# Kernel tuning notes

Hardware: AMD Instinct MI355X
Metric: run time of the kernel (lower is better)

The kernel has to match this reference:

```python
import jax, jax.numpy as jnp
import numpy as np

Q_LEN, KV_LEN, N_HEADS, HEAD_DIM = 2048, 4096, 16, 64
NEG_INF = -1e9


def _causal_prefix_mask(q_len, kv_len):
    # query i (global position prefix+i) may attend to keys j <= prefix + i
    prefix = kv_len - q_len
    i = jnp.arange(q_len)[:, None]
    j = jnp.arange(kv_len)[None, :]
    allowed = j <= (prefix + i)
    return jnp.where(allowed, 0.0, NEG_INF).astype(jnp.float32)[None, None]  # [1,1,q,kv]


def setup_inputs() -> dict:
    key = jax.random.key(0)
    kq, kk, kv = jax.random.split(key, 3)
    query = jax.random.normal(kq, (1, N_HEADS, Q_LEN, HEAD_DIM), dtype=jnp.float32)
    k = jax.random.normal(kk, (1, N_HEADS, KV_LEN, HEAD_DIM), dtype=jnp.float32)
    v = jax.random.normal(kv, (1, N_HEADS, KV_LEN, HEAD_DIM), dtype=jnp.float32)
    attn_mask = _causal_prefix_mask(Q_LEN, KV_LEN)
    return {"query": query, "key": k, "value": v, "attn_mask": attn_mask}


def reference(query, key, value, attn_mask):
    # Equivalent math of SlicedFusedSDPA.forward: chunked causal SDPA with
    # online-softmax merge == one full masked softmax attention.
    # scale=None -> 1/sqrt(head_dim); dropout_p=0; is_causal=True encoded in attn_mask.
    scale = 1.0 / np.sqrt(query.shape[-1]).astype(np.float32)
    scores = jnp.einsum('bhqd,bhkd->bhqk', query, key) * scale + attn_mask  # [B,H,Q,KV]
    probs = jax.nn.softmax(scores, axis=-1)
    out = jnp.einsum('bhqk,bhkd->bhqd', probs, value)
    return out.astype(query.dtype)
```

## Files before the change

kernel.cpp:

```cpp
#include <hip/hip_runtime.h>
#include <hip/hip_bf16.h>

#define NH 16
#define QL 2048
#define KVL 4096
#define DH 64
#define PREFIX (KVL - QL)
#define NT 64
#define TUS 8192
#define NS 2
#define SCALE 0.18033688011112043f

typedef __attribute__((ext_vector_type(8))) _Float16 f16x8;
typedef __attribute__((ext_vector_type(8))) short short8;
typedef __attribute__((ext_vector_type(4))) float f32x4;
typedef __attribute__((ext_vector_type(16))) float f32x16;
typedef unsigned int u32;

static __device__ __forceinline__ float exp2_fast(float x) {
    float r; asm("v_exp_f32 %0, %1" : "=v"(r) : "v"(x)); return r;
}
static __device__ __forceinline__ u32 pkrtz(float lo, float hi) {
    u32 r; asm("v_cvt_pkrtz_f16_f32 %0, %1, %2" : "=v"(r) : "v"(lo), "v"(hi)); return r;
}
static __device__ __forceinline__ void plswap(u32& x, u32& y) {
    asm("v_permlane32_swap_b32 %0, %1" : "+v"(x), "+v"(y));
}
#define MFMAH(a, b, c) __builtin_amdgcn_mfma_f32_32x32x16_f16(a, b, c, 0, 0, 0)

static __device__ __forceinline__ ushort f2bf(float x) {
    union { float f; u32 u; } v; v.f = x;
    u32 r = v.u + 0x7fffu + ((v.u >> 16) & 1u);
    return (ushort)(r >> 16);
}
static __device__ __forceinline__ float bf2f(ushort h) {
    union { u32 u; float f; } v; v.u = ((u32)h) << 16;
    return v.f;
}

__global__ void convK2(const float* __restrict__ K, ushort* __restrict__ ws) {
    const int gid  = blockIdx.x * 256 + threadIdx.x;
    const int lane = gid & 63;
    const int fidx = (gid >> 6) & 7;
    const int tile = (gid >> 9) & 63;
    const int h    = gid >> 15;
    const int lq = lane & 31, hi = lane >> 5;
    const int t = fidx >> 2, ks = fidx & 3;
    const int kv = tile * 64 + t * 32 + lq;
    const float* src = K + ((size_t)h * KVL + kv) * DH + ks * 16 + hi * 8;
    const float4 a = *(const float4*)src;
    const float4 b = *(const float4*)(src + 4);
    const float v[8] = {a.x, a.y, a.z, a.w, b.x, b.y, b.z, b.w};
    f16x8 o;
    #pragma unroll
    for (int j = 0; j < 8; ++j) o[j] = (_Float16)v[j];
    *(f16x8*)(ws + (size_t)(h * NT + tile) * TUS + fidx * 512 + lane * 8) = o;
}

__global__ void convV2(const float* __restrict__ V, ushort* __restrict__ ws) {
    const int gid  = blockIdx.x * 256 + threadIdx.x;
    const int lane = gid & 63;
    const int fidx = (gid >> 6) & 7;
    const int tile = (gid >> 9) & 63;
    const int h    = gid >> 15;
    const int lq = lane & 31, hi = lane >> 5;
    const int dt = fidx >> 2, ks = fidx & 3;
    const int d  = dt * 32 + lq;
    const float* src = V + ((size_t)h * KVL + tile * 64 + ks * 16 + hi * 8) * DH + d;
    f16x8 o;
    #pragma unroll
    for (int j = 0; j < 8; ++j) o[j] = (_Float16)src[j * DH];
    *(f16x8*)(ws + (size_t)(h * NT + tile) * TUS + 4096 + fidx * 512 + lane * 8) = o;
}

__global__ __launch_bounds__(256, 2)
void sdpa_main(const float* __restrict__ Q, const ushort* __restrict__ ws,
               float* __restrict__ part)
{
    const int tid  = threadIdx.x;
    const int lane = tid & 63;
    const int w    = tid >> 6;
    const int lq   = lane & 31;
    const int hi   = lane >> 5;

    const int bid = blockIdx.x;
    const int xcd = bid & 7;
    const int j   = bid >> 3;
    const int h   = xcd * 2 + (j & 1);
    const int qwA = j >> 1;
    const int qw  = (w & 1) ? (63 - qwA) : qwA;
    const int sp  = w >> 1;
    const int qb  = qw * 32;

    const int ntt = (PREFIX + qb + 32 + 63) >> 6;
    const int t0  = (ntt * sp) / NS;
    const int t1  = (ntt * (sp + 1)) / NS;

    f16x8 qh[4], ql[4];
    {
        const float* qp = Q + ((size_t)h * QL + qb + lq) * DH + hi * 8;
        #pragma unroll
        for (int ks = 0; ks < 4; ++ks) {
            const float4 a = *(const float4*)(qp + ks * 16);
            const float4 b = *(const float4*)(qp + ks * 16 + 4);
            const float v[8] = {a.x, a.y, a.z, a.w, b.x, b.y, b.z, b.w};
            #pragma unroll
            for (int jj = 0; jj < 8; ++jj) {
                const float x = v[jj] * SCALE;
                const _Float16 xh = (_Float16)x;
                qh[ks][jj] = xh;
                ql[ks][jj] = (_Float16)(x - (float)xh);
            }
        }
    }

    f32x16 oacc[2];
    #pragma unroll
    for (int dt = 0; dt < 2; ++dt)
        #pragma unroll
        for (int r = 0; r < 16; ++r) oacc[dt][r] = 0.f;
    float m = 0.0f, lsum = 0.f;

    const ushort* tb = ws + (size_t)h * NT * TUS + (size_t)t0 * TUS;

    for (int it = t0; it < t1; ++it, tb += TUS) {
        f16x8 kf[8], vf[8];
        #pragma unroll
        for (int f = 0; f < 8; ++f) kf[f] = *(const f16x8*)(tb + f * 512 + lane * 8);
        #pragma unroll
        for (int f = 0; f < 8; ++f) vf[f] = *(const f16x8*)(tb + 4096 + f * 512 + lane * 8);

        f32x16 sT[2];
        #pragma unroll
        for (int t = 0; t < 2; ++t)
            #pragma unroll
            for (int r = 0; r < 16; ++r) sT[t][r] = 0.f;

        __builtin_amdgcn_s_setprio(1);
        #pragma unroll
        for (int ks = 0; ks < 4; ++ks) {
            sT[0] = MFMAH(kf[ks],     qh[ks], sT[0]);
            sT[1] = MFMAH(kf[4 + ks], qh[ks], sT[1]);
            sT[0] = MFMAH(kf[ks],     ql[ks], sT[0]);
            sT[1] = MFMAH(kf[4 + ks], ql[ks], sT[1]);
        }
        __builtin_amdgcn_s_setprio(0);

        const int kv0 = it * 64;
        if (kv0 + 64 > PREFIX + qb) {
            const int kvlim = PREFIX + qb + lq - kv0;
            #pragma unroll
            for (int t = 0; t < 2; ++t)
                #pragma unroll
                for (int r = 0; r < 16; ++r) {
                    const int kvl = t * 32 + (r & 3) + 8 * (r >> 2) + 4 * hi;
                    if (kvl > kvlim) sT[t][r] = -1e30f;
                }
        }

        float mx = sT[0][0];
        #pragma unroll
        for (int t = 0; t < 2; ++t)
            #pragma unroll
            for (int r = 0; r < 16; ++r) mx = fmaxf(mx, sT[t][r]);
        mx = fmaxf(mx, __shfl_xor(mx, 32));
        if (__any(mx > m + 8.0f)) {
            const float mn  = fmaxf(m, mx);
            const float fsc = exp2_fast(m - mn);
            lsum *= fsc;
            #pragma unroll
            for (int dt = 0; dt < 2; ++dt)
                #pragma unroll
                for (int r = 0; r < 16; ++r) oacc[dt][r] *= fsc;
            m = mn;
        }
        float rs = 0.f;
        #pragma unroll
        for (int t = 0; t < 2; ++t)
            #pragma unroll
            for (int r = 0; r < 16; ++r) {
                const float p = exp2_fast(sT[t][r] - m);
                sT[t][r] = p;
                rs += p;
            }
        lsum += rs;

        f16x8 pb[4];
        #pragma unroll
        for (int t = 0; t < 2; ++t) {
            u32 x0 = pkrtz(sT[t][0],  sT[t][1]);
            u32 x1 = pkrtz(sT[t][2],  sT[t][3]);
            u32 y0 = pkrtz(sT[t][4],  sT[t][5]);
            u32 y1 = pkrtz(sT[t][6],  sT[t][7]);
            u32 x2 = pkrtz(sT[t][8],  sT[t][9]);
            u32 x3 = pkrtz(sT[t][10], sT[t][11]);
            u32 y2 = pkrtz(sT[t][12], sT[t][13]);
            u32 y3 = pkrtz(sT[t][14], sT[t][15]);
            plswap(x0, y0); plswap(x1, y1);
            plswap(x2, y2); plswap(x3, y3);
            union { u32 u[4]; f16x8 v; } p0, p1;
            p0.u[0] = x0; p0.u[1] = x1; p0.u[2] = y0; p0.u[3] = y1;
            p1.u[0] = x2; p1.u[1] = x3; p1.u[2] = y2; p1.u[3] = y3;
            pb[t * 2 + 0] = p0.v;
            pb[t * 2 + 1] = p1.v;
        }

        __builtin_amdgcn_s_setprio(1);
        #pragma unroll
        for (int ks = 0; ks < 4; ++ks) {
            oacc[0] = MFMAH(vf[ks],     pb[ks], oacc[0]);
            oacc[1] = MFMAH(vf[4 + ks], pb[ks], oacc[1]);
        }
        __builtin_amdgcn_s_setprio(0);
    }

    const float ltot = lsum + __shfl_xor(lsum, 32);
    float* pr = part + ((size_t)(sp * NH + h) * QL + qb + lq) * 68;
    #pragma unroll
    for (int dt = 0; dt < 2; ++dt)
        #pragma unroll
        for (int a = 0; a < 4; ++a) {
            f32x4 o;
            #pragma unroll
            for (int jj = 0; jj < 4; ++jj) o[jj] = oacc[dt][a * 4 + jj];
            *(f32x4*)(pr + dt * 32 + a * 8 + hi * 4) = o;
        }
    if (hi == 0) { pr[64] = m; pr[65] = ltot; }
}

__global__ void combine2(const float* __restrict__ part, float* __restrict__ O) {
    const int row = blockIdx.x * 4 + (threadIdx.x >> 6);
    const int d   = threadIdx.x & 63;
    const float* p0 = part + (size_t)row * 68;
    const float* p1 = part + ((size_t)NH * QL + row) * 68;
    const float m0 = p0[64], l0 = p0[65];
    const float m1 = p1[64], l1 = p1[65];
    const float M  = fmaxf(m0, m1);
    const float w0 = exp2f(m0 - M), w1 = exp2f(m1 - M);
    O[(size_t)row * DH + d] = (w0 * p0[d] + w1 * p1[d]) / (w0 * l0 + w1 * l1);
}

#define QT 64
#define KBf 32
#define KSTR 72
#define VSTR 40
#define PSTR 40
#define SCALE_E 0.125f

__global__ __launch_bounds__(256, 2)
void sdpa_fallback(const float* __restrict__ Q, const float* __restrict__ K,
                   const float* __restrict__ V, float* __restrict__ O)
{
    __shared__ ushort sKh[KBf][KSTR];
    __shared__ ushort sKl[KBf][KSTR];
    __shared__ ushort sVt[DH][VSTR];
    __shared__ ushort sPf[4][16][PSTR];

    const int tid  = threadIdx.x;
    const int lane = tid & 63;
    const int w    = tid >> 6;
    const int h    = blockIdx.y;
    const int q0   = blockIdx.x * QT;
    const int qb   = q0 + w * 16;
    const int lrow = lane & 15;
    const int lgrp = lane >> 4;

    short8 qh[2], ql[2];
    {
        const float* qp = Q + ((size_t)h * QL + (qb + lrow)) * DH;
        #pragma unroll
        for (int dh = 0; dh < 2; ++dh) {
            const int d0 = dh * 32 + lgrp * 8;
            #pragma unroll
            for (int jj = 0; jj < 8; ++jj) {
                float x = qp[d0 + jj] * SCALE_E;
                ushort hb = f2bf(x);
                qh[dh][jj] = (short)hb;
                ql[dh][jj] = (short)f2bf(x - bf2f(hb));
            }
        }
    }

    f32x4 oacc[4];
    float m_r[4], l_r[4];
    #pragma unroll
    for (int n = 0; n < 4; ++n) { oacc[n][0]=0.f; oacc[n][1]=0.f; oacc[n][2]=0.f; oacc[n][3]=0.f; }
    #pragma unroll
    for (int r = 0; r < 4; ++r) { m_r[r] = -1e30f; l_r[r] = 0.f; }

    const int nkv = min(KVL, PREFIX + q0 + QT);

    for (int kv0 = 0; kv0 < nkv; kv0 += KBf) {
        __syncthreads();
        {
            const int r  = tid >> 3;
            const int d0 = (tid & 7) * 8;
            const float* kp = K + ((size_t)h * KVL + (kv0 + r)) * DH + d0;
            const float* vp = V + ((size_t)h * KVL + (kv0 + r)) * DH + d0;
            short8 vh, vl;
            #pragma unroll
            for (int jj = 0; jj < 8; ++jj) {
                float x = kp[jj];
                ushort hb = f2bf(x);
                vh[jj] = (short)hb;
                vl[jj] = (short)f2bf(x - bf2f(hb));
            }
            *(short8*)&sKh[r][d0] = vh;
            *(short8*)&sKl[r][d0] = vl;
            #pragma unroll
            for (int jj = 0; jj < 8; ++jj)
                sVt[d0 + jj][r] = f2bf(vp[jj]);
        }
        __syncthreads();

        f32x4 s[2];
        #pragma unroll
        for (int t = 0; t < 2; ++t) { s[t][0]=0.f; s[t][1]=0.f; s[t][2]=0.f; s[t][3]=0.f; }
        #pragma unroll
        for (int t = 0; t < 2; ++t) {
            #pragma unroll
            for (int dh = 0; dh < 2; ++dh) {
                const short8 kh = *(const short8*)&sKh[t*16 + lrow][dh*32 + lgrp*8];
                const short8 kl = *(const short8*)&sKl[t*16 + lrow][dh*32 + lgrp*8];
                s[t] = __builtin_amdgcn_mfma_f32_16x16x32_bf16(qh[dh], kh, s[t], 0, 0, 0);
                s[t] = __builtin_amdgcn_mfma_f32_16x16x32_bf16(qh[dh], kl, s[t], 0, 0, 0);
                s[t] = __builtin_amdgcn_mfma_f32_16x16x32_bf16(ql[dh], kh, s[t], 0, 0, 0);
            }
        }

        if (kv0 + KBf > PREFIX + qb) {
            #pragma unroll
            for (int t = 0; t < 2; ++t)
                #pragma unroll
                for (int r = 0; r < 4; ++r) {
                    const int kv = kv0 + t*16 + lrow;
                    const int q  = qb + lgrp*4 + r;
                    if (kv > PREFIX + q) s[t][r] = -1e30f;
                }
        }

        float tmax[4];
        #pragma unroll
        for (int r = 0; r < 4; ++r) tmax[r] = fmaxf(s[0][r], s[1][r]);
        #pragma unroll
        for (int off = 1; off <= 8; off <<= 1)
            #pragma unroll
            for (int r = 0; r < 4; ++r) tmax[r] = fmaxf(tmax[r], __shfl_xor(tmax[r], off, 64));

        float f[4];
        #pragma unroll
        for (int r = 0; r < 4; ++r) {
            const float mn = fmaxf(m_r[r], tmax[r]);
            f[r] = __expf(m_r[r] - mn);
            m_r[r] = mn;
        }
        #pragma unroll
        for (int t = 0; t < 2; ++t)
            #pragma unroll
            for (int r = 0; r < 4; ++r) s[t][r] = __expf(s[t][r] - m_r[r]);

        float rs[4];
        #pragma unroll
        for (int r = 0; r < 4; ++r) rs[r] = s[0][r] + s[1][r];
        #pragma unroll
        for (int off = 1; off <= 8; off <<= 1)
            #pragma unroll
            for (int r = 0; r < 4; ++r) rs[r] += __shfl_xor(rs[r], off, 64);
        #pragma unroll
        for (int r = 0; r < 4; ++r) l_r[r] = l_r[r] * f[r] + rs[r];
        #pragma unroll
        for (int n = 0; n < 4; ++n)
            #pragma unroll
            for (int r = 0; r < 4; ++r) oacc[n][r] *= f[r];

        #pragma unroll
        for (int t = 0; t < 2; ++t)
            #pragma unroll
            for (int r = 0; r < 4; ++r)
                sPf[w][lgrp*4 + r][t*16 + lrow] = f2bf(s[t][r]);
        asm volatile("s_waitcnt lgkmcnt(0)" ::: "memory");
        __builtin_amdgcn_sched_barrier(0);

        const short8 pa = *(const short8*)&sPf[w][lrow][lgrp*8];
        #pragma unroll
        for (int n = 0; n < 4; ++n) {
            const short8 vb = *(const short8*)&sVt[n*16 + lrow][lgrp*8];
            oacc[n] = __builtin_amdgcn_mfma_f32_16x16x32_bf16(pa, vb, oacc[n], 0, 0, 0);
        }
    }

    float inv[4];
    #pragma unroll
    for (int r = 0; r < 4; ++r) inv[r] = 1.0f / l_r[r];
    float* op = O + ((size_t)h * QL + qb) * DH;
    #pragma unroll
    for (int n = 0; n < 4; ++n)
        #pragma unroll
        for (int r = 0; r < 4; ++r)
            op[(lgrp*4 + r) * DH + n*16 + lrow] = oacc[n][r] * inv[r];
}

extern "C" void kernel_launch(void* const* d_in, const int* in_sizes, int n_in,
                              void* d_out, int out_size, void* d_ws, size_t ws_size,
                              hipStream_t stream) {
    const float* Q = (const float*)d_in[0];
    const float* K = (const float*)d_in[1];
    const float* V = (const float*)d_in[2];
    float* O = (float*)d_out;
    const size_t KVWS = (size_t)NH * NT * TUS * 2;
    const size_t PART = (size_t)NH * QL * 68 * 4;

    if (ws_size >= KVWS + NS * PART) {
        ushort* wsKV = (ushort*)d_ws;
        float*  part = (float*)((char*)d_ws + KVWS);
        hipLaunchKernelGGL(convK2, dim3(2048), dim3(256), 0, stream, K, wsKV);
        hipLaunchKernelGGL(convV2, dim3(2048), dim3(256), 0, stream, V, wsKV);
        hipLaunchKernelGGL(sdpa_main, dim3(512), dim3(256), 0, stream, Q, wsKV, part);
        hipLaunchKernelGGL(combine2, dim3(8192), dim3(256), 0, stream, part, O);
    } else {
        hipLaunchKernelGGL(sdpa_fallback, dim3(32, 16), dim3(256), 0, stream, Q, K, V, O);
    }
}
```

Baseline: 71.69 us.

## Split KV range four ways, merge conversion kernels, tree-reduce softmax max/sum

Templates the main attention kernel on the number of KV splits and launches four splits (1024 blocks) instead of two when workspace allows, with a generalized combine kernel. The K and V fp16 conversion kernels are merged into one launch. Row max and sum reductions become pairwise trees to shorten dependency chains. More splits raise parallelism and balance on the GPU but increase partial-result traffic and combine cost.

Result: slower. 76.34 us (+6.5%).

```diff
diff --git a/kernel.cpp b/kernel.cpp
--- a/kernel.cpp
+++ b/kernel.cpp
@@ -8,7 +8,6 @@
 #define PREFIX (KVL - QL)
 #define NT 64
 #define TUS 8192
-#define NS 2
 #define SCALE 0.18033688011112043f
 
 typedef __attribute__((ext_vector_type(8))) _Float16 f16x8;
@@ -38,41 +37,37 @@
     return v.f;
 }
 
-__global__ void convK2(const float* __restrict__ K, ushort* __restrict__ ws) {
-    const int gid  = blockIdx.x * 256 + threadIdx.x;
+__global__ void convKV(const float* __restrict__ K, const float* __restrict__ V,
+                       ushort* __restrict__ ws) {
+    const int half = blockIdx.x >> 11;
+    const int gid  = (blockIdx.x & 2047) * 256 + threadIdx.x;
     const int lane = gid & 63;
     const int fidx = (gid >> 6) & 7;
     const int tile = (gid >> 9) & 63;
     const int h    = gid >> 15;
     const int lq = lane & 31, hi = lane >> 5;
-    const int t = fidx >> 2, ks = fidx & 3;
-    const int kv = tile * 64 + t * 32 + lq;
-    const float* src = K + ((size_t)h * KVL + kv) * DH + ks * 16 + hi * 8;
-    const float4 a = *(const float4*)src;
-    const float4 b = *(const float4*)(src + 4);
-    const float v[8] = {a.x, a.y, a.z, a.w, b.x, b.y, b.z, b.w};
     f16x8 o;
-    #pragma unroll
-    for (int j = 0; j < 8; ++j) o[j] = (_Float16)v[j];
-    *(f16x8*)(ws + (size_t)(h * NT + tile) * TUS + fidx * 512 + lane * 8) = o;
-}
-
-__global__ void convV2(const float* __restrict__ V, ushort* __restrict__ ws) {
-    const int gid  = blockIdx.x * 256 + threadIdx.x;
-    const int lane = gid & 63;
-    const int fidx = (gid >> 6) & 7;
-    const int tile = (gid >> 9) & 63;
-    const int h    = gid >> 15;
-    const int lq = lane & 31, hi = lane >> 5;
-    const int dt = fidx >> 2, ks = fidx & 3;
-    const int d  = dt * 32 + lq;
-    const float* src = V + ((size_t)h * KVL + tile * 64 + ks * 16 + hi * 8) * DH + d;
-    f16x8 o;
-    #pragma unroll
-    for (int j = 0; j < 8; ++j) o[j] = (_Float16)src[j * DH];
-    *(f16x8*)(ws + (size_t)(h * NT + tile) * TUS + 4096 + fidx * 512 + lane * 8) = o;
-}
-
+    if (half == 0) {
+        const int t = fidx >> 2, ks = fidx & 3;
+        const int kv = tile * 64 + t * 32 + lq;
+        const float* src = K + ((size_t)h * KVL + kv) * DH + ks * 16 + hi * 8;
+        const float4 a = *(const float4*)src;
+        const float4 b = *(const float4*)(src + 4);
+        const float v[8] = {a.x, a.y, a.z, a.w, b.x, b.y, b.z, b.w};
+        #pragma unroll
+        for (int j = 0; j < 8; ++j) o[j] = (_Float16)v[j];
+        *(f16x8*)(ws + (size_t)(h * NT + tile) * TUS + fidx * 512 + lane * 8) = o;
+    } else {
+        const int dt = fidx >> 2, ks = fidx & 3;
+        const int d  = dt * 32 + lq;
+        const float* src = V + ((size_t)h * KVL + tile * 64 + ks * 16 + hi * 8) * DH + d;
+        #pragma unroll
+        for (int j = 0; j < 8; ++j) o[j] = (_Float16)src[j * DH];
+        *(f16x8*)(ws + (size_t)(h * NT + tile) * TUS + 4096 + fidx * 512 + lane * 8) = o;
+    }
+}
+
+template<int NSPLIT>
 __global__ __launch_bounds__(256, 2)
 void sdpa_main(const float* __restrict__ Q, const ushort* __restrict__ ws,
                float* __restrict__ part)
@@ -86,15 +81,22 @@
     const int bid = blockIdx.x;
     const int xcd = bid & 7;
     const int j   = bid >> 3;
-    const int h   = xcd * 2 + (j & 1);
-    const int qwA = j >> 1;
-    const int qw  = (w & 1) ? (63 - qwA) : qwA;
-    const int sp  = w >> 1;
-    const int qb  = qw * 32;
+    int h, qwA, sp;
+    if constexpr (NSPLIT == 4) {
+        h   = xcd * 2 + (j & 1);
+        qwA = j >> 2;
+        sp  = ((j >> 1) & 1) * 2 + (w >> 1);
+    } else {
+        h   = xcd * 2 + (j & 1);
+        qwA = j >> 1;
+        sp  = w >> 1;
+    }
+    const int qw = (w & 1) ? (63 - qwA) : qwA;
+    const int qb = qw * 32;
 
     const int ntt = (PREFIX + qb + 32 + 63) >> 6;
-    const int t0  = (ntt * sp) / NS;
-    const int t1  = (ntt * (sp + 1)) / NS;
+    const int t0  = (ntt * sp) / NSPLIT;
+    const int t1  = (ntt * (sp + 1)) / NSPLIT;
 
     f16x8 qh[4], ql[4];
     {
@@ -158,12 +160,14 @@
                 }
         }
 
-        float mx = sT[0][0];
-        #pragma unroll
-        for (int t = 0; t < 2; ++t)
-            #pragma unroll
-            for (int r = 0; r < 16; ++r) mx = fmaxf(mx, sT[t][r]);
-        mx = fmaxf(mx, __shfl_xor(mx, 32));
+        float tmx[16];
+        #pragma unroll
+        for (int i = 0; i < 16; ++i) tmx[i] = fmaxf(sT[0][i], sT[1][i]);
+        #pragma unroll
+        for (int s = 8; s > 0; s >>= 1)
+            #pragma unroll
+            for (int i = 0; i < s; ++i) tmx[i] = fmaxf(tmx[i], tmx[i + s]);
+        float mx = fmaxf(tmx[0], __shfl_xor(tmx[0], 32));
         if (__any(mx > m + 8.0f)) {
             const float mn  = fmaxf(m, mx);
             const float fsc = exp2_fast(m - mn);
@@ -174,16 +178,18 @@
                 for (int r = 0; r < 16; ++r) oacc[dt][r] *= fsc;
             m = mn;
         }
-        float rs = 0.f;
         #pragma unroll
         for (int t = 0; t < 2; ++t)
             #pragma unroll
-            for (int r = 0; r < 16; ++r) {
-                const float p = exp2_fast(sT[t][r] - m);
-                sT[t][r] = p;
-                rs += p;
-            }
-        lsum += rs;
+            for (int r = 0; r < 16; ++r) sT[t][r] = exp2_fast(sT[t][r] - m);
+        float ts[16];
+        #pragma unroll
+        for (int i = 0; i < 16; ++i) ts[i] = sT[0][i] + sT[1][i];
+        #pragma unroll
+        for (int s = 8; s > 0; s >>= 1)
+            #pragma unroll
+            for (int i = 0; i < s; ++i) ts[i] += ts[i + s];
+        lsum += ts[0];
 
         f16x8 pb[4];
         #pragma unroll
@@ -228,16 +234,26 @@
     if (hi == 0) { pr[64] = m; pr[65] = ltot; }
 }
 
-__global__ void combine2(const float* __restrict__ part, float* __restrict__ O) {
+template<int NSPLIT>
+__global__ void combineN(const float* __restrict__ part, float* __restrict__ O) {
     const int row = blockIdx.x * 4 + (threadIdx.x >> 6);
     const int d   = threadIdx.x & 63;
-    const float* p0 = part + (size_t)row * 68;
-    const float* p1 = part + ((size_t)NH * QL + row) * 68;
-    const float m0 = p0[64], l0 = p0[65];
-    const float m1 = p1[64], l1 = p1[65];
-    const float M  = fmaxf(m0, m1);
-    const float w0 = exp2f(m0 - M), w1 = exp2f(m1 - M);
-    O[(size_t)row * DH + d] = (w0 * p0[d] + w1 * p1[d]) / (w0 * l0 + w1 * l1);
+    float mj[NSPLIT], lj[NSPLIT], M = -1e30f;
+    #pragma unroll
+    for (int j = 0; j < NSPLIT; ++j) {
+        const float* p = part + ((size_t)j * NH * QL + row) * 68;
+        mj[j] = p[64]; lj[j] = p[65];
+        M = fmaxf(M, mj[j]);
+    }
+    float num = 0.f, den = 0.f;
+    #pragma unroll
+    for (int j = 0; j < NSPLIT; ++j) {
+        const float* p = part + ((size_t)j * NH * QL + row) * 68;
+        const float wj = exp2f(mj[j] - M);
+        num += wj * p[d];
+        den += wj * lj[j];
+    }
+    O[(size_t)row * DH + d] = num / den;
 }
 
 #define QT 64
@@ -409,14 +425,17 @@
     float* O = (float*)d_out;
     const size_t KVWS = (size_t)NH * NT * TUS * 2;
     const size_t PART = (size_t)NH * QL * 68 * 4;
-
-    if (ws_size >= KVWS + NS * PART) {
-        ushort* wsKV = (ushort*)d_ws;
-        float*  part = (float*)((char*)d_ws + KVWS);
-        hipLaunchKernelGGL(convK2, dim3(2048), dim3(256), 0, stream, K, wsKV);
-        hipLaunchKernelGGL(convV2, dim3(2048), dim3(256), 0, stream, V, wsKV);
-        hipLaunchKernelGGL(sdpa_main, dim3(512), dim3(256), 0, stream, Q, wsKV, part);
-        hipLaunchKernelGGL(combine2, dim3(8192), dim3(256), 0, stream, part, O);
+    ushort* wsKV = (ushort*)d_ws;
+    float*  part = (float*)((char*)d_ws + KVWS);
+
+    if (ws_size >= KVWS + 4 * PART) {
+        hipLaunchKernelGGL(convKV, dim3(4096), dim3(256), 0, stream, K, V, wsKV);
+        hipLaunchKernelGGL(sdpa_main<4>, dim3(1024), dim3(256), 0, stream, Q, wsKV, part);
+        hipLaunchKernelGGL(combineN<4>, dim3(8192), dim3(256), 0, stream, part, O);
+    } else if (ws_size >= KVWS + 2 * PART) {
+        hipLaunchKernelGGL(convKV, dim3(4096), dim3(256), 0, stream, K, V, wsKV);
+        hipLaunchKernelGGL(sdpa_main<2>, dim3(512), dim3(256), 0, stream, Q, wsKV, part);
+        hipLaunchKernelGGL(combineN<2>, dim3(8192), dim3(256), 0, stream, part, O);
     } else {
         hipLaunchKernelGGL(sdpa_fallback, dim3(32, 16), dim3(256), 0, stream, Q, K, V, O);
     }
```
